# Kernel optimization log

Hardware: AMD Instinct MI355X
Metric: run time of the kernel (lower is better)

The kernel has to match this reference:

```python
import jax, jax.numpy as jnp
import numpy as np

F_OUT = 256      # out_channels
NH = 8           # num_heads
DH = F_OUT // NH # head dim = 32
KH = KW = 8      # kernel (window) size == stride == q_stride
KK = KH * KW     # 64 keys per window


def setup_inputs() -> dict:
    key = jax.random.key(0)
    k1, k2, k3 = jax.random.split(key, 3)
    x = jax.random.normal(k1, (8, 256, 128, 128), jnp.float32)
    # 1x1 conv weight for qkv projection, xavier-ish scale
    proj_w = jax.random.normal(k2, (3 * F_OUT, 256), jnp.float32) * (1.0 / np.sqrt(256.0))
    proj_b = jnp.zeros((3 * F_OUT,), jnp.float32)
    # learned position features (module inits to zeros; use small random for a nontrivial test)
    pos_feats = jax.random.normal(k3, (F_OUT, KK), jnp.float32) * 0.02
    return {"x": x, "proj_w": proj_w, "proj_b": proj_b, "pos_feats": pos_feats}


def reference(x, proj_w, proj_b, pos_feats):
    B, C, H, W = x.shape
    f = F_OUT
    # 1x1 conv == channel GEMM: [B,3f,H,W]
    qkv = jnp.einsum('bchw,oc->bohw', x, proj_w) + proj_b[None, :, None, None]
    scale = float(f // NH) ** (-0.25)
    # query: slice every q_stride-th position -> [B,f,Hq,Wq]
    q = qkv[:, :f, ::KH, ::KW]
    kv = qkv[:, f:3 * f]                       # [B,2f,H,W]
    Hq, Wq = H // KH, W // KW
    # non-overlapping window unfold (stride==kernel, padding=0, dilation=1)
    # -> [B,Hq,Wq,2f,KK], matching torch as_strided(...).reshape(..., -1)
    kv = kv.reshape(B, 2 * f, Hq, KH, Wq, KW)
    kv = kv.transpose(0, 2, 4, 1, 3, 5).reshape(B, Hq, Wq, 2 * f, KK)
    # keys: pos_feats + scale*key, then split heads -> [B,Hq,Wq,NH,DH,KK]
    key_m = (pos_feats + scale * kv[..., :f, :]).reshape(B, Hq, Wq, NH, DH, KK)
    val_m = kv[..., f:2 * f, :].reshape(B, Hq, Wq, NH, DH, KK)
    # queries: scale, channels-last, split heads -> [B,Hq,Wq,NH,DH]
    q_m = (scale * q).transpose(0, 2, 3, 1).reshape(B, Hq, Wq, NH, DH)
    logits = jnp.einsum('bhwnd,bhwndk->bhwnk', q_m, key_m)   # [B,Hq,Wq,NH,KK]
    attn = jax.nn.softmax(logits, axis=-1)
    out = jnp.einsum('bhwnk,bhwndk->bhwnd', attn, val_m)     # [B,Hq,Wq,NH,DH]
    return out.reshape(B, Hq, Wq, f).transpose(0, 3, 1, 2)   # [B,f,Hq,Wq]
```

## Files before the change

kernel.cpp:

```cpp
#include <hip/hip_runtime.h>
#include <hip/hip_bf16.h>
#include <cstdint>
#include <cstddef>

#define SCALE 0.42044820762685725f

typedef __attribute__((ext_vector_type(8))) short short8;
typedef __attribute__((ext_vector_type(4))) short short4v;
typedef __attribute__((ext_vector_type(4))) float f32x4;

__device__ __forceinline__ unsigned int pk2bf(float lo, float hi) {
    __hip_bfloat162 h = __float22bfloat162_rn(float2{lo, hi});
    unsigned int u;
    __builtin_memcpy(&u, &h, sizeof(u));
    return u;
}
__device__ __forceinline__ unsigned short f2bf(float f) {
    unsigned int u = __builtin_bit_cast(unsigned int, f);
    u = (u + 0x7fffu + ((u >> 16) & 1u)) >> 16;
    return (unsigned short)u;
}
__device__ __forceinline__ float bf2f(unsigned short h) {
    unsigned int u = ((unsigned int)h) << 16;
    return __builtin_bit_cast(float, u);
}

__global__ __launch_bounds__(256) void prepack_w(const float* __restrict__ w,
                                                 const float* __restrict__ pos,
                                                 unsigned short* __restrict__ wp,
                                                 unsigned short* __restrict__ pT) {
    int gid = blockIdx.x * 256 + threadIdx.x;
    if (gid < 24576) {
        int lane = gid & 63;
        int ks   = (gid >> 6) & 7;
        int mtg  = gid >> 9;
        int row  = (mtg < 32 ? 256 + mtg * 16 : (mtg - 32) * 16) + (lane & 15);
        int k0   = ks * 32 + (lane >> 4) * 8;
        const float* src = w + row * 256 + k0;
        short8 v;
#pragma unroll
        for (int j = 0; j < 8; ++j) v[j] = (short)f2bf(src[j]);
        *reinterpret_cast<short8*>(wp + (size_t)gid * 8) = v;
    } else {
        int u = gid - 24576;
        pT[u] = f2bf(pos[(u & 255) * 64 + (u >> 8)]);
    }
}

template <bool PRE>
__global__ __launch_bounds__(512, 4) void attn_fused(
        const float* __restrict__ x, const float* __restrict__ proj_w,
        const float* __restrict__ proj_b, const float* __restrict__ pos,
        const unsigned short* __restrict__ wpack, const unsigned short* __restrict__ posT,
        float* __restrict__ out) {
    __shared__ __align__(16) unsigned char s_main[33280];
    __shared__ __align__(16) float s_qs[256];
    __shared__ __align__(16) float s_vbias[256];

    const int t    = threadIdx.x;
    const int lane = t & 63;
    const int wave = t >> 6;
    const int l15  = lane & 15;
    const int l4   = lane >> 4;

    int bid  = blockIdx.x;
    int tile = (bid & 7) * 256 + (bid >> 3);
    int b  = tile >> 8;
    int hq = (tile >> 4) & 15;
    int wq = tile & 15;
    int h0 = hq * 8, w0 = wq * 8;

    const float* xb = x + (size_t)b * 4194304 + (size_t)h0 * 128 + w0;

    if (t < 256) s_vbias[t] = proj_b[512 + t];

    short8 pos8[4];
    if (PRE) {
        const unsigned short* pr = posT + (size_t)lane * 256 + wave * 32;
#pragma unroll
        for (int i = 0; i < 4; ++i)
            pos8[i] = *reinterpret_cast<const short8*>(pr + i * 8);
    }

    {
        const int p   = lane;
        const int pl  = lane & 1;
        const int px0 = lane & ~1;
        const float* xpx = xb + (px0 >> 3) * 128 + (px0 & 7);
        float2 v[16];
#pragma unroll
        for (int g = 0; g < 4; ++g)
#pragma unroll
            for (int j = 0; j < 4; ++j) {
                int c = (g * 8 + wave) * 8 + 2 * j + pl;
                v[g * 4 + j] = *reinterpret_cast<const float2*>(xpx + (size_t)c * 16384);
            }
#pragma unroll
        for (int g = 0; g < 4; ++g) {
            uint4 pk;
            unsigned int* pku = &pk.x;
#pragma unroll
            for (int j = 0; j < 4; ++j) {
                float2 w2 = v[g * 4 + j];
                float sel   = pl ? w2.x : w2.y;
                float other = __shfl_xor(sel, 1);
                pku[j] = pl ? pk2bf(other, w2.y) : pk2bf(w2.x, other);
            }
            int c8 = g * 8 + wave;
            *reinterpret_cast<uint4*>(s_main + p * 512 + ((c8 * 16) ^ ((p & 7) << 4))) = pk;
        }
    }
    __syncthreads();

    f32x4 acc[2][4];
    f32x4 accQ[2];
#pragma unroll
    for (int mt = 0; mt < 2; ++mt) {
        accQ[mt] = (f32x4){0.f, 0.f, 0.f, 0.f};
#pragma unroll
        for (int nt = 0; nt < 4; ++nt) acc[mt][nt] = (f32x4){0.f, 0.f, 0.f, 0.f};
    }

#pragma unroll 2
    for (int ks = 0; ks < 8; ++ks) {
        short8 bfr[4];
#pragma unroll
        for (int nt = 0; nt < 4; ++nt) {
            int n  = nt * 16 + l15;
            int kb = ks * 32 + l4 * 8;
            bfr[nt] = *reinterpret_cast<const short8*>(
                s_main + n * 512 + ((2 * kb) ^ ((n & 7) << 4)));
        }
        short8 afk[2], afq[2];
#pragma unroll
        for (int mt = 0; mt < 2; ++mt) {
            if (PRE) {
                afk[mt] = *reinterpret_cast<const short8*>(
                    wpack + ((size_t)(((wave * 2 + mt) * 8 + ks) * 64 + lane)) * 8);
                afq[mt] = *reinterpret_cast<const short8*>(
                    wpack + ((size_t)(((32 + wave * 2 + mt) * 8 + ks) * 64 + lane)) * 8);
            } else {
                const float* wk = proj_w + (256 + (wave * 2 + mt) * 16 + l15) * 256 + ks * 32 + l4 * 8;
                const float* wq2 = proj_w + ((wave * 2 + mt) * 16 + l15) * 256 + ks * 32 + l4 * 8;
#pragma unroll
                for (int j = 0; j < 8; ++j) { afk[mt][j] = (short)f2bf(wk[j]); afq[mt][j] = (short)f2bf(wq2[j]); }
            }
        }
#pragma unroll
        for (int mt = 0; mt < 2; ++mt)
#pragma unroll
            for (int nt = 0; nt < 4; ++nt)
                acc[mt][nt] = __builtin_amdgcn_mfma_f32_16x16x32_bf16(afk[mt], bfr[nt], acc[mt][nt], 0, 0, 0);
#pragma unroll
        for (int mt = 0; mt < 2; ++mt)
            accQ[mt] = __builtin_amdgcn_mfma_f32_16x16x32_bf16(afq[mt], bfr[0], accQ[mt], 0, 0, 0);
    }

    if (l15 == 0) {
#pragma unroll
        for (int mt = 0; mt < 2; ++mt)
#pragma unroll
            for (int i = 0; i < 4; ++i) {
                int row = wave * 32 + mt * 16 + l4 * 4 + i;
                s_qs[row] = SCALE * (accQ[mt][i] + proj_b[row]);
            }
    }

    unsigned int kpk[2][4][2];
#pragma unroll
    for (int mt = 0; mt < 2; ++mt)
#pragma unroll
        for (int nt = 0; nt < 4; ++nt) {
            kpk[mt][nt][0] = pk2bf(acc[mt][nt][0], acc[mt][nt][1]);
            kpk[mt][nt][1] = pk2bf(acc[mt][nt][2], acc[mt][nt][3]);
        }

#pragma unroll
    for (int mt = 0; mt < 2; ++mt)
#pragma unroll
        for (int nt = 0; nt < 4; ++nt) acc[mt][nt] = (f32x4){0.f, 0.f, 0.f, 0.f};
#pragma unroll 2
    for (int ks = 0; ks < 8; ++ks) {
        short8 bfr[4];
#pragma unroll
        for (int nt = 0; nt < 4; ++nt) {
            int n  = nt * 16 + l15;
            int kb = ks * 32 + l4 * 8;
            bfr[nt] = *reinterpret_cast<const short8*>(
                s_main + n * 512 + ((2 * kb) ^ ((n & 7) << 4)));
        }
        short8 afv[2];
#pragma unroll
        for (int mt = 0; mt < 2; ++mt) {
            if (PRE) {
                afv[mt] = *reinterpret_cast<const short8*>(
                    wpack + ((size_t)(((16 + wave * 2 + mt) * 8 + ks) * 64 + lane)) * 8);
            } else {
                const float* wv = proj_w + (512 + (wave * 2 + mt) * 16 + l15) * 256 + ks * 32 + l4 * 8;
#pragma unroll
                for (int j = 0; j < 8; ++j) afv[mt][j] = (short)f2bf(wv[j]);
            }
        }
#pragma unroll
        for (int mt = 0; mt < 2; ++mt)
#pragma unroll
            for (int nt = 0; nt < 4; ++nt)
                acc[mt][nt] = __builtin_amdgcn_mfma_f32_16x16x32_bf16(afv[mt], bfr[nt], acc[mt][nt], 0, 0, 0);
    }

    __syncthreads();

#pragma unroll
    for (int mt = 0; mt < 2; ++mt) {
        int m0 = wave * 32 + mt * 16 + l4 * 4;
#pragma unroll
        for (int nt = 0; nt < 4; ++nt) {
            int k = nt * 16 + l15;
            uint2 w2; w2.x = kpk[mt][nt][0]; w2.y = kpk[mt][nt][1];
            *reinterpret_cast<uint2*>(s_main + k * 520 + ((2 * m0) ^ (nt << 3))) = w2;
        }
    }

    float attnw;
    {
        const int k  = lane;
        const int xv = ((k >> 4) & 3) << 3;
        const unsigned char* krow = s_main + (size_t)k * 520;
        float lg = 0.f;
#pragma unroll
        for (int d4 = 0; d4 < 8; ++d4) {
            short4v kv = *reinterpret_cast<const short4v*>(
                krow + ((2 * (wave * 32 + d4 * 4)) ^ xv));
#pragma unroll
            for (int u = 0; u < 4; ++u) {
                const int d = d4 * 4 + u;
                float q = s_qs[wave * 32 + d];
                float pf = PRE ? bf2f((unsigned short)pos8[d >> 3][d & 7])
                               : pos[(size_t)(wave * 32 + d) * 64 + k];
                lg = fmaf(q, fmaf(SCALE, bf2f((unsigned short)kv[u]), pf), lg);
            }
        }
        float mx = lg;
#pragma unroll
        for (int off = 32; off >= 1; off >>= 1) mx = fmaxf(mx, __shfl_xor(mx, off));
        float e = __expf(lg - mx);
        float s = e;
#pragma unroll
        for (int off = 32; off >= 1; off >>= 1) s += __shfl_xor(s, off);
        attnw = e / s;
    }

    {
        float a0 = __shfl(attnw, l15);
        float a1 = __shfl(attnw, 16 + l15);
        float a2 = __shfl(attnw, 32 + l15);
        float a3 = __shfl(attnw, 48 + l15);
#pragma unroll
        for (int mt = 0; mt < 2; ++mt) {
#pragma unroll
            for (int i = 0; i < 4; ++i) {
                float sum = a0 * acc[mt][0][i] + a1 * acc[mt][1][i]
                          + a2 * acc[mt][2][i] + a3 * acc[mt][3][i];
                sum += __shfl_xor(sum, 1);
                sum += __shfl_xor(sum, 2);
                sum += __shfl_xor(sum, 4);
                sum += __shfl_xor(sum, 8);
                if (l15 == 0) {
                    int vr = wave * 32 + mt * 16 + l4 * 4 + i;
                    out[(size_t)b * 65536 + (size_t)vr * 256 + hq * 16 + wq] = sum + s_vbias[vr];
                }
            }
        }
    }
}

extern "C" void kernel_launch(void* const* d_in, const int* in_sizes, int n_in,
                              void* d_out, int out_size, void* d_ws, size_t ws_size,
                              hipStream_t stream) {
    (void)in_sizes; (void)n_in; (void)out_size;
    const float* x      = (const float*)d_in[0];
    const float* proj_w = (const float*)d_in[1];
    const float* proj_b = (const float*)d_in[2];
    const float* pos    = (const float*)d_in[3];
    float* out = (float*)d_out;

    const size_t need_ws = 393216 + 32768;
    if (d_ws != nullptr && ws_size >= need_ws) {
        unsigned short* wp = (unsigned short*)d_ws;
        unsigned short* pT = (unsigned short*)((char*)d_ws + 393216);
        prepack_w<<<160, 256, 0, stream>>>(proj_w, pos, wp, pT);
        attn_fused<true><<<2048, 512, 0, stream>>>(x, proj_w, proj_b, pos, wp, pT, out);
    } else {
        attn_fused<false><<<2048, 512, 0, stream>>>(x, proj_w, proj_b, pos, nullptr, nullptr, out);
    }
}
```

Measured before the change: 92.58 us.

## Move query projection to separate kernel and compute logits from MFMA registers

Query projection moves to a new FP32 kernel that writes per-tile scaled queries to workspace, so the fused kernel no longer issues wasted Q MFMAs on a 16-column tile. The fused kernel now runs the K and V GEMMs in one loop with doubled accumulators. It computes logits directly from the K accumulator registers using shuffles, removing the bf16 repack of K, the LDS transpose round-trip and a barrier. In exchange it adds an extra kernel launch, higher register pressure from 64 accumulator floats, and global reads of positional features per lane.

```diff
diff --git a/kernel.cpp b/kernel.cpp
--- a/kernel.cpp
+++ b/kernel.cpp
@@ -25,10 +25,12 @@
     return __builtin_bit_cast(float, u);
 }
 
+
 __global__ __launch_bounds__(256) void prepack_w(const float* __restrict__ w,
                                                  const float* __restrict__ pos,
                                                  unsigned short* __restrict__ wp,
-                                                 unsigned short* __restrict__ pT) {
+                                                 unsigned short* __restrict__ pT,
+                                                 float* __restrict__ wqT) {
     int gid = blockIdx.x * 256 + threadIdx.x;
     if (gid < 24576) {
         int lane = gid & 63;
@@ -41,10 +43,40 @@
 #pragma unroll
         for (int j = 0; j < 8; ++j) v[j] = (short)f2bf(src[j]);
         *reinterpret_cast<short8*>(wp + (size_t)gid * 8) = v;
-    } else {
+    } else if (gid < 40960) {
         int u = gid - 24576;
         pT[u] = f2bf(pos[(u & 255) * 64 + (u >> 8)]);
-    }
+    } else {
+        int u = gid - 40960;
+        wqT[u] = w[(u & 255) * 256 + (u >> 8)];
+    }
+}
+
+__global__ __launch_bounds__(256) void q_kernel(const float* __restrict__ x,
+                                                const float* __restrict__ wqT,
+                                                const float* __restrict__ proj_b,
+                                                float* __restrict__ q_all) {
+    __shared__ float s_x0[4][256];
+    const int t = threadIdx.x;
+    const int tile0 = blockIdx.x * 4;
+    const int b = tile0 >> 8, hq = (tile0 >> 4) & 15, wq0 = tile0 & 15;
+    {
+        const float* src = x + (size_t)b * 4194304 + (size_t)t * 16384 + hq * 1024 + wq0 * 8;
+#pragma unroll
+        for (int j = 0; j < 4; ++j) s_x0[j][t] = src[j * 8];
+    }
+    __syncthreads();
+    float acc[4] = {0.f, 0.f, 0.f, 0.f};
+#pragma unroll 8
+    for (int c = 0; c < 256; ++c) {
+        float wv = wqT[c * 256 + t];
+#pragma unroll
+        for (int j = 0; j < 4; ++j) acc[j] = fmaf(wv, s_x0[j][c], acc[j]);
+    }
+    float bq = proj_b[t];
+#pragma unroll
+    for (int j = 0; j < 4; ++j)
+        q_all[(size_t)(tile0 + j) * 256 + t] = SCALE * (acc[j] + bq);
 }
 
 template <bool PRE>
@@ -52,10 +84,10 @@
         const float* __restrict__ x, const float* __restrict__ proj_w,
         const float* __restrict__ proj_b, const float* __restrict__ pos,
         const unsigned short* __restrict__ wpack, const unsigned short* __restrict__ posT,
-        float* __restrict__ out) {
-    __shared__ __align__(16) unsigned char s_main[33280];
+        const float* __restrict__ q_all, float* __restrict__ out) {
+    __shared__ __align__(16) unsigned char s_main[32768];
+    __shared__ __align__(16) float s_vbias[256];
     __shared__ __align__(16) float s_qs[256];
-    __shared__ __align__(16) float s_vbias[256];
 
     const int t    = threadIdx.x;
     const int lane = t & 63;
@@ -68,19 +100,10 @@
     int b  = tile >> 8;
     int hq = (tile >> 4) & 15;
     int wq = tile & 15;
-    int h0 = hq * 8, w0 = wq * 8;
-
-    const float* xb = x + (size_t)b * 4194304 + (size_t)h0 * 128 + w0;
+
+    const float* xb = x + (size_t)b * 4194304 + (size_t)(hq * 8) * 128 + wq * 8;
 
     if (t < 256) s_vbias[t] = proj_b[512 + t];
-
-    short8 pos8[4];
-    if (PRE) {
-        const unsigned short* pr = posT + (size_t)lane * 256 + wave * 32;
-#pragma unroll
-        for (int i = 0; i < 4; ++i)
-            pos8[i] = *reinterpret_cast<const short8*>(pr + i * 8);
-    }
 
     {
         const int p   = lane;
@@ -112,13 +135,15 @@
     }
     __syncthreads();
 
-    f32x4 acc[2][4];
+    f32x4 acc[4][4];
+#pragma unroll
+    for (int mt = 0; mt < 4; ++mt)
+#pragma unroll
+        for (int nt = 0; nt < 4; ++nt) acc[mt][nt] = (f32x4){0.f, 0.f, 0.f, 0.f};
     f32x4 accQ[2];
-#pragma unroll
-    for (int mt = 0; mt < 2; ++mt) {
-        accQ[mt] = (f32x4){0.f, 0.f, 0.f, 0.f};
-#pragma unroll
-        for (int nt = 0; nt < 4; ++nt) acc[mt][nt] = (f32x4){0.f, 0.f, 0.f, 0.f};
+    if (!PRE) {
+#pragma unroll
+        for (int mt = 0; mt < 2; ++mt) accQ[mt] = (f32x4){0.f, 0.f, 0.f, 0.f};
     }
 
 #pragma unroll 2
@@ -131,144 +156,123 @@
             bfr[nt] = *reinterpret_cast<const short8*>(
                 s_main + n * 512 + ((2 * kb) ^ ((n & 7) << 4)));
         }
-        short8 afk[2], afq[2];
+        short8 afk[2], afv[2];
 #pragma unroll
         for (int mt = 0; mt < 2; ++mt) {
             if (PRE) {
                 afk[mt] = *reinterpret_cast<const short8*>(
                     wpack + ((size_t)(((wave * 2 + mt) * 8 + ks) * 64 + lane)) * 8);
-                afq[mt] = *reinterpret_cast<const short8*>(
-                    wpack + ((size_t)(((32 + wave * 2 + mt) * 8 + ks) * 64 + lane)) * 8);
-            } else {
-                const float* wk = proj_w + (256 + (wave * 2 + mt) * 16 + l15) * 256 + ks * 32 + l4 * 8;
-                const float* wq2 = proj_w + ((wave * 2 + mt) * 16 + l15) * 256 + ks * 32 + l4 * 8;
-#pragma unroll
-                for (int j = 0; j < 8; ++j) { afk[mt][j] = (short)f2bf(wk[j]); afq[mt][j] = (short)f2bf(wq2[j]); }
-            }
-        }
-#pragma unroll
-        for (int mt = 0; mt < 2; ++mt)
-#pragma unroll
-            for (int nt = 0; nt < 4; ++nt)
-                acc[mt][nt] = __builtin_amdgcn_mfma_f32_16x16x32_bf16(afk[mt], bfr[nt], acc[mt][nt], 0, 0, 0);
-#pragma unroll
-        for (int mt = 0; mt < 2; ++mt)
-            accQ[mt] = __builtin_amdgcn_mfma_f32_16x16x32_bf16(afq[mt], bfr[0], accQ[mt], 0, 0, 0);
-    }
-
-    if (l15 == 0) {
-#pragma unroll
-        for (int mt = 0; mt < 2; ++mt)
-#pragma unroll
-            for (int i = 0; i < 4; ++i) {
-                int row = wave * 32 + mt * 16 + l4 * 4 + i;
-                s_qs[row] = SCALE * (accQ[mt][i] + proj_b[row]);
-            }
-    }
-
-    unsigned int kpk[2][4][2];
-#pragma unroll
-    for (int mt = 0; mt < 2; ++mt)
-#pragma unroll
-        for (int nt = 0; nt < 4; ++nt) {
-            kpk[mt][nt][0] = pk2bf(acc[mt][nt][0], acc[mt][nt][1]);
-            kpk[mt][nt][1] = pk2bf(acc[mt][nt][2], acc[mt][nt][3]);
-        }
-
-#pragma unroll
-    for (int mt = 0; mt < 2; ++mt)
-#pragma unroll
-        for (int nt = 0; nt < 4; ++nt) acc[mt][nt] = (f32x4){0.f, 0.f, 0.f, 0.f};
-#pragma unroll 2
-    for (int ks = 0; ks < 8; ++ks) {
-        short8 bfr[4];
-#pragma unroll
-        for (int nt = 0; nt < 4; ++nt) {
-            int n  = nt * 16 + l15;
-            int kb = ks * 32 + l4 * 8;
-            bfr[nt] = *reinterpret_cast<const short8*>(
-                s_main + n * 512 + ((2 * kb) ^ ((n & 7) << 4)));
-        }
-        short8 afv[2];
-#pragma unroll
-        for (int mt = 0; mt < 2; ++mt) {
-            if (PRE) {
                 afv[mt] = *reinterpret_cast<const short8*>(
                     wpack + ((size_t)(((16 + wave * 2 + mt) * 8 + ks) * 64 + lane)) * 8);
             } else {
+                const float* wk = proj_w + (256 + (wave * 2 + mt) * 16 + l15) * 256 + ks * 32 + l4 * 8;
                 const float* wv = proj_w + (512 + (wave * 2 + mt) * 16 + l15) * 256 + ks * 32 + l4 * 8;
 #pragma unroll
-                for (int j = 0; j < 8; ++j) afv[mt][j] = (short)f2bf(wv[j]);
+                for (int j = 0; j < 8; ++j) { afk[mt][j] = (short)f2bf(wk[j]); afv[mt][j] = (short)f2bf(wv[j]); }
             }
         }
 #pragma unroll
         for (int mt = 0; mt < 2; ++mt)
 #pragma unroll
+            for (int nt = 0; nt < 4; ++nt) {
+                acc[mt][nt]     = __builtin_amdgcn_mfma_f32_16x16x32_bf16(afk[mt], bfr[nt], acc[mt][nt], 0, 0, 0);
+                acc[2 + mt][nt] = __builtin_amdgcn_mfma_f32_16x16x32_bf16(afv[mt], bfr[nt], acc[2 + mt][nt], 0, 0, 0);
+            }
+        if (!PRE) {
+            short8 afq[2];
+#pragma unroll
+            for (int mt = 0; mt < 2; ++mt) {
+                const float* wq2 = proj_w + ((wave * 2 + mt) * 16 + l15) * 256 + ks * 32 + l4 * 8;
+#pragma unroll
+                for (int j = 0; j < 8; ++j) afq[mt][j] = (short)f2bf(wq2[j]);
+                accQ[mt] = __builtin_amdgcn_mfma_f32_16x16x32_bf16(afq[mt], bfr[0], accQ[mt], 0, 0, 0);
+            }
+        }
+    }
+
+    if (!PRE) {
+        if (l15 == 0) {
+#pragma unroll
+            for (int mt = 0; mt < 2; ++mt)
+#pragma unroll
+                for (int i = 0; i < 4; ++i) {
+                    int row = wave * 32 + mt * 16 + l4 * 4 + i;
+                    s_qs[row] = SCALE * (accQ[mt][i] + proj_b[row]);
+                }
+        }
+    }
+
+    float attnw[4];
+    {
+        float qf[2][4];
+        if (PRE) {
+            const float* qp = q_all + (size_t)tile * 256 + wave * 32 + l4 * 4;
+#pragma unroll
+            for (int mt = 0; mt < 2; ++mt) {
+                float4 qv = *reinterpret_cast<const float4*>(qp + mt * 16);
+                qf[mt][0] = qv.x; qf[mt][1] = qv.y; qf[mt][2] = qv.z; qf[mt][3] = qv.w;
+            }
+        } else {
+#pragma unroll
+            for (int mt = 0; mt < 2; ++mt)
+#pragma unroll
+                for (int i = 0; i < 4; ++i) qf[mt][i] = s_qs[wave * 32 + mt * 16 + l4 * 4 + i];
+        }
+        short4v pos4[4][2];
+        if (PRE) {
+#pragma unroll
             for (int nt = 0; nt < 4; ++nt)
-                acc[mt][nt] = __builtin_amdgcn_mfma_f32_16x16x32_bf16(afv[mt], bfr[nt], acc[mt][nt], 0, 0, 0);
-    }
-
-    __syncthreads();
+#pragma unroll
+                for (int mt = 0; mt < 2; ++mt)
+                    pos4[nt][mt] = *reinterpret_cast<const short4v*>(
+                        posT + (size_t)(nt * 16 + l15) * 256 + wave * 32 + mt * 16 + l4 * 4);
+        }
+
+        float lg[4];
+#pragma unroll
+        for (int nt = 0; nt < 4; ++nt) {
+            float p = 0.f;
+#pragma unroll
+            for (int mt = 0; mt < 2; ++mt)
+#pragma unroll
+                for (int i = 0; i < 4; ++i) {
+                    float pf = PRE ? bf2f((unsigned short)pos4[nt][mt][i])
+                                   : pos[(size_t)(wave * 32 + mt * 16 + l4 * 4 + i) * 64 + nt * 16 + l15];
+                    p = fmaf(qf[mt][i], fmaf(SCALE, acc[mt][nt][i], pf), p);
+                }
+            p += __shfl_xor(p, 16);
+            p += __shfl_xor(p, 32);
+            lg[nt] = p;
+        }
+        float mx = fmaxf(fmaxf(lg[0], lg[1]), fmaxf(lg[2], lg[3]));
+        mx = fmaxf(mx, __shfl_xor(mx, 1));
+        mx = fmaxf(mx, __shfl_xor(mx, 2));
+        mx = fmaxf(mx, __shfl_xor(mx, 4));
+        mx = fmaxf(mx, __shfl_xor(mx, 8));
+        float e0 = __expf(lg[0] - mx), e1 = __expf(lg[1] - mx);
+        float e2 = __expf(lg[2] - mx), e3 = __expf(lg[3] - mx);
+        float s = (e0 + e1) + (e2 + e3);
+        s += __shfl_xor(s, 1);
+        s += __shfl_xor(s, 2);
+        s += __shfl_xor(s, 4);
+        s += __shfl_xor(s, 8);
+        float rs = 1.f / s;
+        attnw[0] = e0 * rs; attnw[1] = e1 * rs; attnw[2] = e2 * rs; attnw[3] = e3 * rs;
+    }
 
 #pragma unroll
     for (int mt = 0; mt < 2; ++mt) {
-        int m0 = wave * 32 + mt * 16 + l4 * 4;
-#pragma unroll
-        for (int nt = 0; nt < 4; ++nt) {
-            int k = nt * 16 + l15;
-            uint2 w2; w2.x = kpk[mt][nt][0]; w2.y = kpk[mt][nt][1];
-            *reinterpret_cast<uint2*>(s_main + k * 520 + ((2 * m0) ^ (nt << 3))) = w2;
-        }
-    }
-
-    float attnw;
-    {
-        const int k  = lane;
-        const int xv = ((k >> 4) & 3) << 3;
-        const unsigned char* krow = s_main + (size_t)k * 520;
-        float lg = 0.f;
-#pragma unroll
-        for (int d4 = 0; d4 < 8; ++d4) {
-            short4v kv = *reinterpret_cast<const short4v*>(
-                krow + ((2 * (wave * 32 + d4 * 4)) ^ xv));
-#pragma unroll
-            for (int u = 0; u < 4; ++u) {
-                const int d = d4 * 4 + u;
-                float q = s_qs[wave * 32 + d];
-                float pf = PRE ? bf2f((unsigned short)pos8[d >> 3][d & 7])
-                               : pos[(size_t)(wave * 32 + d) * 64 + k];
-                lg = fmaf(q, fmaf(SCALE, bf2f((unsigned short)kv[u]), pf), lg);
-            }
-        }
-        float mx = lg;
-#pragma unroll
-        for (int off = 32; off >= 1; off >>= 1) mx = fmaxf(mx, __shfl_xor(mx, off));
-        float e = __expf(lg - mx);
-        float s = e;
-#pragma unroll
-        for (int off = 32; off >= 1; off >>= 1) s += __shfl_xor(s, off);
-        attnw = e / s;
-    }
-
-    {
-        float a0 = __shfl(attnw, l15);
-        float a1 = __shfl(attnw, 16 + l15);
-        float a2 = __shfl(attnw, 32 + l15);
-        float a3 = __shfl(attnw, 48 + l15);
-#pragma unroll
-        for (int mt = 0; mt < 2; ++mt) {
-#pragma unroll
-            for (int i = 0; i < 4; ++i) {
-                float sum = a0 * acc[mt][0][i] + a1 * acc[mt][1][i]
-                          + a2 * acc[mt][2][i] + a3 * acc[mt][3][i];
-                sum += __shfl_xor(sum, 1);
-                sum += __shfl_xor(sum, 2);
-                sum += __shfl_xor(sum, 4);
-                sum += __shfl_xor(sum, 8);
-                if (l15 == 0) {
-                    int vr = wave * 32 + mt * 16 + l4 * 4 + i;
-                    out[(size_t)b * 65536 + (size_t)vr * 256 + hq * 16 + wq] = sum + s_vbias[vr];
-                }
+#pragma unroll
+        for (int i = 0; i < 4; ++i) {
+            float sum = attnw[0] * acc[2 + mt][0][i] + attnw[1] * acc[2 + mt][1][i]
+                      + attnw[2] * acc[2 + mt][2][i] + attnw[3] * acc[2 + mt][3][i];
+            sum += __shfl_xor(sum, 1);
+            sum += __shfl_xor(sum, 2);
+            sum += __shfl_xor(sum, 4);
+            sum += __shfl_xor(sum, 8);
+            if (l15 == 0) {
+                int vr = wave * 32 + mt * 16 + l4 * 4 + i;
+                out[(size_t)b * 65536 + (size_t)vr * 256 + hq * 16 + wq] = sum + s_vbias[vr];
             }
         }
     }
@@ -284,13 +288,20 @@
     const float* pos    = (const float*)d_in[3];
     float* out = (float*)d_out;
 
-    const size_t need_ws = 393216 + 32768;
+    const size_t OFF_POST = 393216;
+    const size_t OFF_WQT  = 425984;
+    const size_t OFF_QALL = 688128;
+    const size_t need_ws  = OFF_QALL + 2097152;
+
     if (d_ws != nullptr && ws_size >= need_ws) {
-        unsigned short* wp = (unsigned short*)d_ws;
-        unsigned short* pT = (unsigned short*)((char*)d_ws + 393216);
-        prepack_w<<<160, 256, 0, stream>>>(proj_w, pos, wp, pT);
-        attn_fused<true><<<2048, 512, 0, stream>>>(x, proj_w, proj_b, pos, wp, pT, out);
+        unsigned short* wp  = (unsigned short*)d_ws;
+        unsigned short* pT  = (unsigned short*)((char*)d_ws + OFF_POST);
+        float*          wqT = (float*)((char*)d_ws + OFF_WQT);
+        float*          qA  = (float*)((char*)d_ws + OFF_QALL);
+        prepack_w<<<416, 256, 0, stream>>>(proj_w, pos, wp, pT, wqT);
+        q_kernel<<<512, 256, 0, stream>>>(x, wqT, proj_b, qA);
+        attn_fused<true><<<2048, 512, 0, stream>>>(x, proj_w, proj_b, pos, wp, pT, qA, out);
     } else {
-        attn_fused<false><<<2048, 512, 0, stream>>>(x, proj_w, proj_b, pos, nullptr, nullptr, out);
-    }
-}
+        attn_fused<false><<<2048, 512, 0, stream>>>(x, proj_w, proj_b, pos, nullptr, nullptr, nullptr, out);
+    }
+}
```

Result: faster. 85.44 us (-7.7%).
